# Kernel tuning notes

Hardware: AMD Instinct MI355X
Metric: run time of the kernel (lower is better)

Reference implementation:

```python
import jax, jax.numpy as jnp
import numpy as np

B = 8192
IN = 512          # inputs feature dim (input_size[2])
CTX = 256         # context_input_size
CENTER = 512      # center_size
MIN_ = IN + CTX   # module_input_size = 768
FF = 1024         # n_ff_pre_units
RNN = 1024        # n_rnn_units
OUT = 512         # output_size
O2C = 256         # output_to_center_size
TOT = OUT + O2C   # total_output_size = 768


def setup_inputs() -> dict:
    key = jax.random.key(0)
    ks = jax.random.split(key, 12)
    return {
        "inputs": jax.random.normal(ks[0], (B, 1, IN), jnp.float32),
        "center_state": jax.random.normal(ks[1], (B, 1, CENTER), jnp.float32),
        "module_state": jax.random.normal(ks[2], (B, 1, RNN), jnp.float32),
        # reading_weights: truncated normal stddev 0.1 in TF; plain normal*0.1 is fine for a math reference
        "W_read": jax.random.normal(ks[3], (CENTER, CTX), jnp.float32) * 0.1,
        "W_pre": jax.random.normal(ks[4], (MIN_, FF), jnp.float32) * (1.0 / np.sqrt(MIN_)),
        "b_pre": jnp.zeros((FF,), jnp.float32),
        "Wx": jax.random.normal(ks[5], (FF, RNN), jnp.float32) * (1.0 / np.sqrt(FF)),
        "Wh": jax.random.normal(ks[6], (RNN, RNN), jnp.float32) * (1.0 / np.sqrt(RNN)),
        "b_rnn": jnp.zeros((RNN,), jnp.float32),
        "W_post": jax.random.normal(ks[7], (RNN, TOT), jnp.float32) * (1.0 / np.sqrt(RNN)),
        "b_post": jnp.zeros((TOT,), jnp.float32),
    }


def reference(inputs, center_state, module_state, W_read, W_pre, b_pre, Wx, Wh, b_rnn, W_post, b_post):
    # tf.clip_by_norm(W, 1.0): global Frobenius norm clip
    norm = jnp.sqrt(jnp.sum(W_read * W_read))
    W_clip = W_read * (1.0 / jnp.maximum(norm, 1.0))
    # context read: [B,1,CENTER] @ [CENTER,CTX] -> [B,1,CTX]
    context = jnp.einsum("btc,cd->btd", center_state, W_clip)
    module_inputs = jnp.concatenate([inputs, context], axis=2)  # [B,1,MIN_]
    rnn_in = jax.nn.relu(jnp.einsum("btf,fg->btg", module_inputs, W_pre) + b_pre)
    # SimpleRNNCell: h' = tanh(x Wx + h Wh + b)
    h_new = jnp.tanh(jnp.einsum("btf,fg->btg", rnn_in, Wx)
                     + jnp.einsum("btf,fg->btg", module_state, Wh) + b_rnn)
    module_output = jax.nn.relu(jnp.einsum("btf,fg->btg", h_new, W_post) + b_post)
    network_output = module_output[:, :, :OUT]
    module_output_to_center = module_output[:, :, OUT:]
    return (network_output, module_output_to_center, h_new)
```

## Files before the change

### kernel.cpp

```cpp
#include <hip/hip_runtime.h>

typedef __bf16 bf16x8 __attribute__((ext_vector_type(8)));
typedef float  f32x4  __attribute__((ext_vector_type(4)));
typedef unsigned short ushort8 __attribute__((ext_vector_type(8)));

#define B_ROWS 8192
#define OUT_D  512
#define O2C_D  256
#define TOT_D  768
#define MIN_D  768
#define RNN_D  1024

__device__ __forceinline__ unsigned short f2bf(float f) {
    unsigned int u = __builtin_bit_cast(unsigned int, f);
    u = (u + 0x7fff + ((u >> 16) & 1)) >> 16;
    return (unsigned short)u;
}

__device__ __forceinline__ void load_lds16(const void* g, void* l) {
    __builtin_amdgcn_global_load_lds(
        (const __attribute__((address_space(1))) unsigned int*)g,
        (__attribute__((address_space(3))) unsigned int*)l, 16, 0, 0);
}

__launch_bounds__(256)
__global__ void prep_all(const float* __restrict__ Wread, float* __restrict__ partials,
                         const float* __restrict__ Wpre, const float* __restrict__ Wx,
                         const float* __restrict__ Wh,  const float* __restrict__ Wpost,
                         unsigned short* __restrict__ WpreT, unsigned short* __restrict__ WxhT,
                         unsigned short* __restrict__ WpostT, unsigned short* __restrict__ WreadT,
                         const float* __restrict__ center, const float* __restrict__ inputs,
                         const float* __restrict__ mstate,
                         unsigned short* __restrict__ csB, unsigned short* __restrict__ miB,
                         unsigned short* __restrict__ rnB) {
    const int bid = blockIdx.x;
    const int tid = threadIdx.x;
    if (bid < 128) {
        __shared__ float red[4];
        const float* p = Wread + bid * 1024 + tid * 4;
        f32x4 v = *(const f32x4*)p;
        float s = v[0]*v[0] + v[1]*v[1] + v[2]*v[2] + v[3]*v[3];
        #pragma unroll
        for (int off = 32; off > 0; off >>= 1) s += __shfl_down(s, off, 64);
        if ((tid & 63) == 0) red[tid >> 6] = s;
        __syncthreads();
        if (tid == 0) partials[bid] = red[0] + red[1] + red[2] + red[3];
        return;
    }
    if (bid < 1984) {
        int g = (bid - 128) * 256 + tid;
        const float* W; unsigned short* out; int N, ostride;
        if (g < 98304)        { W = Wpre;  out = WpreT;        N = 1024; ostride = 768;  }
        else if (g < 229376)  { g -= 98304;  W = Wx;    out = WxhT;        N = 1024; ostride = 2048; }
        else if (g < 360448)  { g -= 229376; W = Wh;    out = WxhT + 1024; N = 1024; ostride = 2048; }
        else if (g < 458752)  { g -= 360448; W = Wpost; out = WpostT;      N = 768;  ostride = 1024; }
        else                  { g -= 458752; W = Wread; out = WreadT;      N = 256;  ostride = 512;  }
        int n  = g % N;
        int kg = g / N;
        ushort8 o;
        #pragma unroll
        for (int j = 0; j < 8; ++j)
            o[j] = f2bf(W[(long)(kg * 8 + j) * N + n]);
        *(ushort8*)(out + (long)n * ostride + kg * 8) = o;
        return;
    }
    long g = (long)(bid - 1984) * 256 + tid;
    const float* src; unsigned short* dst; int logc, ostride;
    if (g < 524288)       { src = center; dst = csB;        logc = 9;  ostride = 512;  }
    else if (g < 1048576) { g -= 524288;  src = inputs; dst = miB;        logc = 9;  ostride = 768;  }
    else                  { g -= 1048576; src = mstate; dst = rnB + 1024; logc = 10; ostride = 2048; }
    long e = g * 8;
    long row = e >> logc;
    int  col = (int)(e & ((1 << logc) - 1));
    f32x4 v0 = *(const f32x4*)(src + e);
    f32x4 v1 = *(const f32x4*)(src + e + 4);
    ushort8 o;
    o[0] = f2bf(v0[0]); o[1] = f2bf(v0[1]); o[2] = f2bf(v0[2]); o[3] = f2bf(v0[3]);
    o[4] = f2bf(v1[0]); o[5] = f2bf(v1[1]); o[6] = f2bf(v1[2]); o[7] = f2bf(v1[3]);
    *(ushort8*)(dst + row * (long)ostride + col) = o;
}

template<int MODE, int BNT>
__launch_bounds__(256, 4)
__global__ void gemm_bt(const unsigned short* __restrict__ A,
                        const unsigned short* __restrict__ Bt,
                        int K, const float* __restrict__ bias,
                        unsigned short* __restrict__ outB, int ldob,
                        float* __restrict__ outF, int ldof) {
    constexpr int U   = BNT / 32;
    constexpr int BJ  = BNT / 32;
    __shared__ alignas(16) unsigned short smem[128 * 64 + BNT * 64];
    unsigned short* sA = smem;
    unsigned short* sB = smem + 128 * 64;

    const int tid  = threadIdx.x;
    const int wave = tid >> 6;
    const int lane = tid & 63;
    const int bm = blockIdx.x, bn = blockIdx.y;
    const int wm = wave & 1, wn = wave >> 1;
    const int lr = lane >> 4;
    const int lc = lane & 15;
    const int sw = lc & 7;

    f32x4 acc[4][U] = {};

    long aoff[4], boff[BJ];
    #pragma unroll
    for (int j = 0; j < 4; ++j) {
        const int c   = tid + j * 256;
        const int row = c >> 3;
        const int kg  = (c & 7) ^ (row & 7);
        aoff[j] = (long)(bm * 128 + row) * K + kg * 8;
    }
    #pragma unroll
    for (int j = 0; j < BJ; ++j) {
        const int c   = tid + j * 256;
        const int row = c >> 3;
        const int kg  = (c & 7) ^ (row & 7);
        boff[j] = (long)(bn * BNT + row) * K + kg * 8;
    }

    for (int k0 = 0; k0 < K; k0 += 64) {
        #pragma unroll
        for (int j = 0; j < 4; ++j)
            load_lds16(A + aoff[j] + k0, (char*)sA + j * 4096 + wave * 1024);
        #pragma unroll
        for (int j = 0; j < BJ; ++j)
            load_lds16(Bt + boff[j] + k0, (char*)sB + j * 4096 + wave * 1024);
        __syncthreads();

        #pragma unroll
        for (int kh = 0; kh < 2; ++kh) {
            const int ch = (kh * 4 + lr) ^ sw;
            bf16x8 af[4], bfr[U];
            #pragma unroll
            for (int t = 0; t < 4; ++t)
                af[t] = *(const bf16x8*)(sA + (wm * 64 + t * 16 + lc) * 64 + ch * 8);
            #pragma unroll
            for (int u = 0; u < U; ++u)
                bfr[u] = *(const bf16x8*)(sB + (wn * (BNT / 2) + u * 16 + lc) * 64 + ch * 8);
            #pragma unroll
            for (int i = 0; i < 4; ++i)
                #pragma unroll
                for (int u = 0; u < U; ++u)
                    acc[i][u] = __builtin_amdgcn_mfma_f32_16x16x32_bf16(af[i], bfr[u], acc[i][u], 0, 0, 0);
        }
        __syncthreads();
    }

    float sc = 1.f;
    if constexpr (MODE == 0) {
        float s = 0.f;
        for (int i = 0; i < 128; ++i) s += bias[i];
        sc = 1.f / fmaxf(sqrtf(s), 1.f);
    }
    #pragma unroll
    for (int u = 0; u < U; ++u) {
        float bv = 0.f;
        if constexpr (MODE != 0) bv = bias[bn * BNT + wn * (BNT / 2) + u * 16 + lc];
        #pragma unroll
        for (int tm = 0; tm < 4; ++tm)
            #pragma unroll
            for (int r = 0; r < 4; ++r) {
                float v = acc[tm][u][r];
                if constexpr (MODE == 0) v *= sc;
                else v += bv;
                if constexpr (MODE == 1 || MODE == 3) v = fmaxf(v, 0.f);
                if constexpr (MODE == 2) v = tanhf(v);
                acc[tm][u][r] = v;
            }
    }

    const int ctcol = wn * (BNT / 2);

    if constexpr (MODE <= 2) {
        unsigned short* Cb = smem;
        #pragma unroll
        for (int u = 0; u < U; ++u)
            #pragma unroll
            for (int tm = 0; tm < 4; ++tm)
                #pragma unroll
                for (int r = 0; r < 4; ++r)
                    Cb[(wm * 64 + tm * 16 + lr * 4 + r) * BNT + ctcol + u * 16 + lc] =
                        f2bf(acc[tm][u][r]);
        __syncthreads();
        constexpr int RC = BNT / 8;
        constexpr int CPT = 128 * RC / 256;
        #pragma unroll
        for (int t = 0; t < CPT; ++t) {
            const int chunk = t * 256 + tid;
            const int row = chunk / RC;
            const int c8  = chunk % RC;
            ushort8 val = *(ushort8*)(Cb + row * BNT + c8 * 8);
            *(ushort8*)(outB + (long)(bm * 128 + row) * ldob + bn * BNT + c8 * 8) = val;
        }
    }

    if constexpr (MODE == 2 || MODE == 3) {
        float* Cf = (float*)smem;
        #pragma unroll
        for (int h = 0; h < 2; ++h) {
            __syncthreads();
            if (wm == h) {
                #pragma unroll
                for (int u = 0; u < U; ++u)
                    #pragma unroll
                    for (int tm = 0; tm < 4; ++tm)
                        #pragma unroll
                        for (int r = 0; r < 4; ++r)
                            Cf[(tm * 16 + lr * 4 + r) * BNT + ctcol + u * 16 + lc] =
                                acc[tm][u][r];
            }
            __syncthreads();
            constexpr int RCF = BNT / 4;
            constexpr int CPTF = 64 * RCF / 256;
            #pragma unroll
            for (int t = 0; t < CPTF; ++t) {
                const int chunk = t * 256 + tid;
                const int row = chunk / RCF;
                const int c4  = chunk % RCF;
                f32x4 val = *(f32x4*)(Cf + row * BNT + c4 * 4);
                const long grow = bm * 128 + h * 64 + row;
                if constexpr (MODE == 2) {
                    *(f32x4*)(outF + grow * ldof + bn * BNT + c4 * 4) = val;
                } else {
                    if (bn * BNT < OUT_D)
                        *(f32x4*)(outF + grow * OUT_D + bn * BNT + c4 * 4) = val;
                    else
                        *(f32x4*)(outF + (long)B_ROWS * OUT_D + grow * O2C_D
                                  + (bn * BNT - OUT_D) + c4 * 4) = val;
                }
            }
        }
    }
}

extern "C" void kernel_launch(void* const* d_in, const int* in_sizes, int n_in,
                              void* d_out, int out_size, void* d_ws, size_t ws_size,
                              hipStream_t stream) {
    const float* inputs = (const float*)d_in[0];
    const float* center = (const float*)d_in[1];
    const float* mstate = (const float*)d_in[2];
    const float* W_read = (const float*)d_in[3];
    const float* W_pre  = (const float*)d_in[4];
    const float* b_pre  = (const float*)d_in[5];
    const float* Wx     = (const float*)d_in[6];
    const float* Wh     = (const float*)d_in[7];
    const float* b_rnn  = (const float*)d_in[8];
    const float* W_post = (const float*)d_in[9];
    const float* b_post = (const float*)d_in[10];
    float* out = (float*)d_out;

    char* ws = (char*)d_ws;
    float* partials = (float*)ws;
    unsigned short* WreadT = (unsigned short*)(ws + 1024);
    unsigned short* WpreT  = WreadT + 256 * 512;
    unsigned short* WxhT   = WpreT  + 1024 * 768;
    unsigned short* WpostT = WxhT   + (long)1024 * 2048;
    unsigned short* csB    = WpostT + 768 * 1024;
    unsigned short* miB    = csB + (long)B_ROWS * 512;
    unsigned short* rnB    = miB + (long)B_ROWS * MIN_D;
    unsigned short* hB     = rnB + (long)B_ROWS * 2048;

    prep_all<<<10176, 256, 0, stream>>>(W_read, partials,
                                        W_pre, Wx, Wh, W_post,
                                        WpreT, WxhT, WpostT, WreadT,
                                        center, inputs, mstate, csB, miB, rnB);

    gemm_bt<0, 64><<<dim3(64, 4), 256, 0, stream>>>(csB, WreadT, 512, partials,
                                                    miB + 512, MIN_D, nullptr, 0);
    gemm_bt<1, 128><<<dim3(64, 8), 256, 0, stream>>>(miB, WpreT, 768, b_pre,
                                                     rnB, 2048, nullptr, 0);
    gemm_bt<2, 128><<<dim3(64, 8), 256, 0, stream>>>(rnB, WxhT, 2048, b_rnn,
                                                     hB, RNN_D,
                                                     out + (long)B_ROWS * TOT_D, RNN_D);
    gemm_bt<3, 128><<<dim3(64, 6), 256, 0, stream>>>(hB, WpostT, 1024, b_post,
                                                     nullptr, 0, out, 0);
}
```

Before: 248.3 us.

## Use dedicated 256x128-tile triple-buffered GEMM for RNN step, retile post GEMM

Adds a new 512-thread kernel computing the RNN GEMM (K=2048) with 256x128 output tiles, a three-stage LDS buffer fed by direct global-to-LDS loads, split-K-half MFMA phases and setprio scheduling, fused bias+tanh and dual bf16/fp32 stores. The larger tile increases operand reuse per block and the deeper pipeline hides load latency. The post-GEMM is relaunched with 64-wide N tiles to raise block count. The larger tile halves the number of blocks for the RNN GEMM (256 blocks), which may leave some compute units idle.

```diff
diff --git a/kernel.cpp b/kernel.cpp
--- a/kernel.cpp
+++ b/kernel.cpp
@@ -166,7 +166,6 @@
                 if constexpr (MODE == 0) v *= sc;
                 else v += bv;
                 if constexpr (MODE == 1 || MODE == 3) v = fmaxf(v, 0.f);
-                if constexpr (MODE == 2) v = tanhf(v);
                 acc[tm][u][r] = v;
             }
     }
@@ -196,7 +195,7 @@
         }
     }
 
-    if constexpr (MODE == 2 || MODE == 3) {
+    if constexpr (MODE == 3) {
         float* Cf = (float*)smem;
         #pragma unroll
         for (int h = 0; h < 2; ++h) {
@@ -221,17 +220,179 @@
                 const int c4  = chunk % RCF;
                 f32x4 val = *(f32x4*)(Cf + row * BNT + c4 * 4);
                 const long grow = bm * 128 + h * 64 + row;
-                if constexpr (MODE == 2) {
-                    *(f32x4*)(outF + grow * ldof + bn * BNT + c4 * 4) = val;
-                } else {
-                    if (bn * BNT < OUT_D)
-                        *(f32x4*)(outF + grow * OUT_D + bn * BNT + c4 * 4) = val;
-                    else
-                        *(f32x4*)(outF + (long)B_ROWS * OUT_D + grow * O2C_D
-                                  + (bn * BNT - OUT_D) + c4 * 4) = val;
-                }
+                if (bn * BNT < OUT_D)
+                    *(f32x4*)(outF + grow * OUT_D + bn * BNT + c4 * 4) = val;
+                else
+                    *(f32x4*)(outF + (long)B_ROWS * OUT_D + grow * O2C_D
+                              + (bn * BNT - OUT_D) + c4 * 4) = val;
             }
         }
+    }
+}
+
+__launch_bounds__(512, 1)
+__global__ void gemm256(const unsigned short* __restrict__ A,
+                        const unsigned short* __restrict__ Bt,
+                        int K, const float* __restrict__ bias,
+                        unsigned short* __restrict__ outB,
+                        float* __restrict__ outF) {
+    constexpr int ABUF = 256 * 64;
+    constexpr int BBUF = 128 * 64;
+    constexpr int BUFE = ABUF + BBUF;
+    __shared__ alignas(16) unsigned short smem[3 * BUFE];
+
+    const int tid  = threadIdx.x;
+    const int wave = tid >> 6;
+    const int lane = tid & 63;
+    const int bn = blockIdx.x, bm = blockIdx.y;
+    const int wm = wave >> 1, wn = wave & 1;
+    const int lr = lane >> 4;
+    const int lc = lane & 15;
+    const int sw = lc & 7;
+    const int nt = K >> 6;
+
+    f32x4 acc[4][4] = {};
+
+    long aoff[4], boff[2];
+    #pragma unroll
+    for (int j = 0; j < 4; ++j) {
+        const int c   = tid + j * 512;
+        const int row = c >> 3;
+        const int kg  = (c & 7) ^ (row & 7);
+        aoff[j] = (long)(bm * 256 + row) * K + kg * 8;
+    }
+    #pragma unroll
+    for (int j = 0; j < 2; ++j) {
+        const int c   = tid + j * 512;
+        const int row = c >> 3;
+        const int kg  = (c & 7) ^ (row & 7);
+        boff[j] = (long)(bn * 128 + row) * K + kg * 8;
+    }
+
+    auto stageA2 = [&](int buf, int k0, int jlo) {
+        char* base = (char*)(smem + buf * BUFE);
+        load_lds16(A + aoff[jlo]     + k0, base + jlo       * 8192 + wave * 1024);
+        load_lds16(A + aoff[jlo + 1] + k0, base + (jlo + 1) * 8192 + wave * 1024);
+    };
+    auto stageB1 = [&](int buf, int k0, int j) {
+        char* base = (char*)(smem + buf * BUFE) + ABUF * 2;
+        load_lds16(Bt + boff[j] + k0, base + j * 8192 + wave * 1024);
+    };
+    auto dsA = [&](int buf, int kh, bf16x8* af) {
+        const unsigned short* sA = smem + buf * BUFE;
+        const int ch = (kh * 4 + lr) ^ sw;
+        #pragma unroll
+        for (int m = 0; m < 4; ++m)
+            af[m] = *(const bf16x8*)(sA + (wm * 64 + m * 16 + lc) * 64 + ch * 8);
+    };
+    auto dsB = [&](int buf, int kh, bf16x8* bf) {
+        const unsigned short* sB = smem + buf * BUFE + ABUF;
+        const int ch = (kh * 4 + lr) ^ sw;
+        #pragma unroll
+        for (int n = 0; n < 4; ++n)
+            bf[n] = *(const bf16x8*)(sB + (wn * 64 + n * 16 + lc) * 64 + ch * 8);
+    };
+
+    stageA2(0, 0, 0); stageA2(0, 0, 2); stageB1(0, 0, 0); stageB1(0, 0, 1);
+    if (nt > 1) {
+        stageA2(1, 64, 0); stageA2(1, 64, 2); stageB1(1, 64, 0); stageB1(1, 64, 1);
+        asm volatile("s_waitcnt vmcnt(6)" ::: "memory");
+    } else {
+        asm volatile("s_waitcnt vmcnt(0)" ::: "memory");
+    }
+    __builtin_amdgcn_s_barrier();
+
+    int cur = 0;
+    for (int t = 0; t < nt; ++t) {
+        const int  k2   = (t + 2) << 6;
+        const bool st   = (t + 2) < nt;
+        const int  nbuf = (cur >= 1) ? cur - 1 : cur + 2;
+
+        bf16x8 af[4], bf[4];
+
+        if (st) { stageA2(nbuf, k2, 0); stageB1(nbuf, k2, 0); }
+        dsA(cur, 0, af); dsB(cur, 0, bf);
+        __builtin_amdgcn_s_barrier();
+        asm volatile("s_waitcnt lgkmcnt(0)" ::: "memory");
+        __builtin_amdgcn_sched_barrier(0);
+        __builtin_amdgcn_s_setprio(1);
+        #pragma unroll
+        for (int m = 0; m < 4; ++m)
+            #pragma unroll
+            for (int n = 0; n < 4; ++n)
+                acc[m][n] = __builtin_amdgcn_mfma_f32_16x16x32_bf16(af[m], bf[n], acc[m][n], 0, 0, 0);
+        __builtin_amdgcn_s_setprio(0);
+        __builtin_amdgcn_s_barrier();
+
+        if (st) { stageA2(nbuf, k2, 2); stageB1(nbuf, k2, 1); }
+        dsA(cur, 1, af); dsB(cur, 1, bf);
+        if (t + 1 < nt) {
+            if (st) asm volatile("s_waitcnt vmcnt(6)" ::: "memory");
+            else    asm volatile("s_waitcnt vmcnt(0)" ::: "memory");
+        }
+        __builtin_amdgcn_s_barrier();
+        asm volatile("s_waitcnt lgkmcnt(0)" ::: "memory");
+        __builtin_amdgcn_sched_barrier(0);
+        __builtin_amdgcn_s_setprio(1);
+        #pragma unroll
+        for (int m = 0; m < 4; ++m)
+            #pragma unroll
+            for (int n = 0; n < 4; ++n)
+                acc[m][n] = __builtin_amdgcn_mfma_f32_16x16x32_bf16(af[m], bf[n], acc[m][n], 0, 0, 0);
+        __builtin_amdgcn_s_setprio(0);
+        __builtin_amdgcn_s_barrier();
+
+        cur = (cur == 2) ? 0 : cur + 1;
+    }
+
+    #pragma unroll
+    for (int n = 0; n < 4; ++n) {
+        const float bv = bias[bn * 128 + wn * 64 + n * 16 + lc];
+        #pragma unroll
+        for (int m = 0; m < 4; ++m)
+            #pragma unroll
+            for (int r = 0; r < 4; ++r)
+                acc[m][n][r] = tanhf(acc[m][n][r] + bv);
+    }
+
+    unsigned short* Cb = smem;
+    __syncthreads();
+    #pragma unroll
+    for (int m = 0; m < 4; ++m)
+        #pragma unroll
+        for (int n = 0; n < 4; ++n)
+            #pragma unroll
+            for (int r = 0; r < 4; ++r)
+                Cb[(wm * 64 + m * 16 + lr * 4 + r) * 128 + wn * 64 + n * 16 + lc] =
+                    f2bf(acc[m][n][r]);
+    __syncthreads();
+    #pragma unroll
+    for (int tch = 0; tch < 8; ++tch) {
+        const int chunk = tch * 512 + tid;
+        const int row = chunk >> 4;
+        const int c8  = chunk & 15;
+        ushort8 v = *(ushort8*)(Cb + row * 128 + c8 * 8);
+        *(ushort8*)(outB + (long)(bm * 256 + row) * RNN_D + bn * 128 + c8 * 8) = v;
+    }
+    __syncthreads();
+
+    float* Cf = (float*)smem;
+    #pragma unroll
+    for (int m = 0; m < 4; ++m)
+        #pragma unroll
+        for (int n = 0; n < 4; ++n)
+            #pragma unroll
+            for (int r = 0; r < 4; ++r)
+                Cf[(wm * 64 + m * 16 + lr * 4 + r) * 128 + wn * 64 + n * 16 + lc] =
+                    acc[m][n][r];
+    __syncthreads();
+    #pragma unroll
+    for (int tch = 0; tch < 16; ++tch) {
+        const int chunk = tch * 512 + tid;
+        const int row = chunk >> 5;
+        const int c4  = chunk & 31;
+        f32x4 v = *(f32x4*)(Cf + row * 128 + c4 * 4);
+        *(f32x4*)(outF + (long)(bm * 256 + row) * RNN_D + bn * 128 + c4 * 4) = v;
     }
 }
 
@@ -271,9 +432,8 @@
                                                     miB + 512, MIN_D, nullptr, 0);
     gemm_bt<1, 128><<<dim3(64, 8), 256, 0, stream>>>(miB, WpreT, 768, b_pre,
                                                      rnB, 2048, nullptr, 0);
-    gemm_bt<2, 128><<<dim3(64, 8), 256, 0, stream>>>(rnB, WxhT, 2048, b_rnn,
-                                                     hB, RNN_D,
-                                                     out + (long)B_ROWS * TOT_D, RNN_D);
-    gemm_bt<3, 128><<<dim3(64, 6), 256, 0, stream>>>(hB, WpostT, 1024, b_post,
+    gemm256<<<dim3(8, 32), 512, 0, stream>>>(rnB, WxhT, 2048, b_rnn,
+                                             hB, out + (long)B_ROWS * TOT_D);
+    gemm_bt<3, 64><<<dim3(64, 12), 256, 0, stream>>>(hB, WpostT, 1024, b_post,
                                                      nullptr, 0, out, 0);
 }
```

After: 241.2 us. -2.9%, faster.
